# Kernel optimization log

Measured on AMD Instinct MI355X. Metric: run time of the kernel, lower is better.

Reference implementation:

```python
import jax, jax.numpy as jnp
import numpy as np

T, B, NS, NC = 100, 4096, 12, 4
N = NS + NC  # tau dim


def setup_inputs() -> dict:
    key = jax.random.key(0)
    k1, k2, k3, k4, k5 = jax.random.split(key, 5)
    # Symmetric PD quadratic cost C = L L^T / N + I  -> well conditioned
    L = jax.random.normal(k1, (T, B, N, N), dtype=jnp.float32) * 0.1
    C = jnp.einsum('tbij,tbkj->tbik', L, L) + jnp.eye(N, dtype=jnp.float32)
    c = jax.random.normal(k2, (T, B, N), dtype=jnp.float32)
    # Linear dynamics x' = F [x;u] + f, state block near identity for stability
    F = jax.random.normal(k3, (T - 1, B, NS, N), dtype=jnp.float32) * 0.02
    A0 = jnp.concatenate([0.99 * jnp.eye(NS, dtype=jnp.float32),
                          jnp.zeros((NS, NC), jnp.float32)], axis=-1)
    F = F + A0  # broadcast over (T-1, B)
    f = jax.random.normal(k4, (T - 1, B, NS), dtype=jnp.float32) * 0.01
    x_init = jax.random.normal(k5, (B, NS), dtype=jnp.float32)
    return {"x_init": x_init, "C": C, "c": c, "F": F, "f": f}


def _lqr_solve(x_init, C, c, F, f):
    ns = x_init.shape[-1]
    # Pad dynamics to length T (terminal step has no dynamics; V starts at 0
    # so the padded zero F/f contribute nothing).
    Fp = jnp.concatenate([F, jnp.zeros_like(F[:1])], axis=0)  # [T,B,ns,n]
    fp = jnp.concatenate([f, jnp.zeros_like(f[:1])], axis=0)  # [T,B,ns]

    def bwd_step(carry, inp):
        V, v = carry                      # [B,ns,ns], [B,ns]
        Ct, ct, Ft, ft = inp
        # Q = C + F^T V F ; q = c + F^T (V f + v)
        Q = Ct + jnp.einsum('bsi,bst,btj->bij', Ft, V, Ft)
        Vf = jnp.einsum('bst,bt->bs', V, ft) + v
        q = ct + jnp.einsum('bsi,bs->bi', Ft, Vf)
        Qxx, Qxu = Q[:, :ns, :ns], Q[:, :ns, ns:]
        Qux, Quu = Q[:, ns:, :ns], Q[:, ns:, ns:]
        qx, qu = q[:, :ns], q[:, ns:]
        # Joint solve for K = -Quu^{-1} Qux, k = -Quu^{-1} qu
        Kk = -jnp.linalg.solve(Quu, jnp.concatenate([Qux, qu[..., None]], axis=-1))
        K, k = Kk[..., :ns], Kk[..., ns]
        Vn = Qxx + jnp.einsum('bij,bjk->bik', Qxu, K)
        Vn = 0.5 * (Vn + jnp.swapaxes(Vn, -1, -2))
        vn = qx + jnp.einsum('bij,bj->bi', Qxu, k)
        return (Vn, vn), (K, k)

    V0 = jnp.zeros((x_init.shape[0], ns, ns), C.dtype)
    v0 = jnp.zeros((x_init.shape[0], ns), C.dtype)
    _, (Kr, kr) = jax.lax.scan(bwd_step, (V0, v0),
                               (C[::-1], c[::-1], Fp[::-1], fp[::-1]))
    K, k = Kr[::-1], kr[::-1]  # [T,B,nc,ns], [T,B,nc]

    def fwd_step(x, inp):
        Ct, ct, Ft, ft, Kt, kt = inp
        u = jnp.einsum('bij,bj->bi', Kt, x) + kt
        tau = jnp.concatenate([x, u], axis=-1)
        cost = 0.5 * jnp.einsum('bi,bij,bj->b', tau, Ct, tau) \
               + jnp.einsum('bi,bi->b', ct, tau)
        xn = jnp.einsum('bij,bj->bi', Ft, tau) + ft
        return xn, (x, u, cost)

    _, (xs, us, costs) = jax.lax.scan(fwd_step, x_init, (C, c, Fp, fp, K, k))
    return xs, us, jnp.sum(costs, axis=0)


def reference(x_init, C, c, F, f):
    # MPC with QuadCost + LinDx and no box constraints: the iLQR loop
    # converges in one exact LQR solve (Riccati backward + forward rollout).
    x, u, objs = _lqr_solve(x_init, C, c, F, f)
    return x, u, objs
```

## Files before the change

### kernel.cpp

```cpp
#include <hip/hip_runtime.h>
#include <hip/hip_fp16.h>

#define TT 100
#define BB 4096
#define GS 648


#define FENCE() asm volatile("s_waitcnt lgkmcnt(0)" ::: "memory")

template<int KMODE>
__device__ __forceinline__ void storeK(void* wsv, size_t of, int l, float X0,float X1,float X2,float X3){
  if (KMODE==0){
    float* wsb=(float*)wsv + of*52;
    if (l<12)       ((float4*)wsb)[l]  = make_float4(X0,X1,X2,X3);
    else if (l==12) ((float4*)wsb)[12] = make_float4(X0,X1,X2,X3);
  } else {
    __half* wsb=(__half*)wsv + of*52;
    if (l<12){
      wsb[l*4+0]=__float2half(X0); wsb[l*4+1]=__float2half(X1);
      wsb[l*4+2]=__float2half(X2); wsb[l*4+3]=__float2half(X3);
    } else if (l==12){
      wsb[48]=__float2half(X0); wsb[49]=__float2half(X1);
      wsb[50]=__float2half(X2); wsb[51]=__float2half(X3);
    }
  }
}
template<int KMODE>
__device__ __forceinline__ float4 loadKcol(const void* wsv, size_t of, int l){
  if (KMODE==0) return ((const float4*)((const float*)wsv + of*52))[l];
  const __half* p=(const __half*)wsv + of*52 + l*4;
  return make_float4(__half2float(p[0]),__half2float(p[1]),__half2float(p[2]),__half2float(p[3]));
}
template<int KMODE>
__device__ __forceinline__ float loadkk(const void* wsv, size_t of, int r){
  if (KMODE==0) return ((const float*)wsv)[of*52+48+r];
  return __half2float(((const __half*)wsv)[of*52+48+r]);
}

template<int KMODE>
__global__ __launch_bounds__(256)
void lqr_fused(const float* __restrict__ xinit,
               const float* __restrict__ Cg,
               const float* __restrict__ cg,
               const float* __restrict__ Fg,
               const float* __restrict__ fg,
               float* __restrict__ out,
               void* __restrict__ wsv)
{
  __shared__ float smem[GS*8];
  const int tid  = threadIdx.x;
  const int gi   = tid >> 5;
  const int lane = tid & 63;
  const int l    = tid & 15;
  const int h    = (tid >> 4) & 1;
  const int b    = blockIdx.x*8 + gi;
  const int gb32 = lane & ~31;

  float* __restrict__ V   = smem + gi*GS;
  float* __restrict__ Fl  = V + 144;
  float* __restrict__ S   = V + 384;
  float* __restrict__ Qxu = V + 528;
  float* __restrict__ Quu = V + 576;
  float* __restrict__ vv  = V + 592;
  float* __restrict__ tb  = V + 604;

  if (h==0 && l<12){
    #pragma unroll
    for (int i=0;i<12;i++) V[i*12+l]=0.f;
    vv[l]=0.f;
  }

  float4 sCa,sCb; float sc_;
  float4 sFa=make_float4(0,0,0,0),sFb=sFa; float sf_=0.f;
  {
    const size_t of = ((size_t)(TT-1)*BB + b);
    const float4* pc = (const float4*)(Cg + of*256 + l*16);
    sCa=pc[2*h]; sCb=pc[2*h+1];
    sc_ = cg[of*16 + l];
  }

  for (int tt=TT-1; tt>=0; --tt){
    const bool hasF = (tt < TT-1);
    float4 Ca=sCa,Cb=sCb; float rc=sc_;
    float4 Fa=sFa,Fb=sFb; float rf=sf_;

    if (hasF && l<12){
      float4* q=(float4*)(Fl + l*20);
      q[2*h]=Fa; q[2*h+1]=Fb;
      if (h==0) tb[l]=rf;
    }
    FENCE();

    if (tt>0){
      const size_t of = ((size_t)(tt-1)*BB + b);
      const float4* pc=(const float4*)(Cg + of*256 + l*16);
      sCa=pc[2*h]; sCb=pc[2*h+1];
      sc_=cg[of*16+l];
      if (l<12){
        const float4* pf=(const float4*)(Fg + of*192 + l*16);
        sFa=pf[2*h]; sFb=pf[2*h+1];
        if (h==0) sf_=fg[of*12+l];
      }
    }

    const float R0=Ca.x,R1=Ca.y,R2=Ca.z,R3=Ca.w,R4=Cb.x,R5=Cb.y,R6=Cb.z,R7=Cb.w;
    float Qp[16];
    Qp[0]=h?0.f:R0; Qp[1]=h?0.f:R1; Qp[2]=h?0.f:R2; Qp[3]=h?0.f:R3;
    Qp[4]=h?0.f:R4; Qp[5]=h?0.f:R5; Qp[6]=h?0.f:R6; Qp[7]=h?0.f:R7;
    Qp[8]=h?R0:0.f; Qp[9]=h?R1:0.f; Qp[10]=h?R2:0.f; Qp[11]=h?R3:0.f;
    Qp[12]=h?R4:0.f; Qp[13]=h?R5:0.f; Qp[14]=h?R6:0.f; Qp[15]=h?R7:0.f;
    float qvp = h? 0.f : rc;

    if (hasF){
      float FtL[6], FtH[6];
      #pragma unroll
      for (int k2=0;k2<6;k2++){ FtL[k2]=Fl[k2*20+l]; FtH[k2]=Fl[(6+k2)*20+l]; }
      const int s0=6*h;
      float Wl[6];
      #pragma unroll
      for (int k2=0;k2<6;k2++){
        const float4* vr=(const float4*)(V+(s0+k2)*12);
        float4 v0=vr[0],v1=vr[1],v2=vr[2];
        Wl[k2]= v0.x*FtL[0]+v0.y*FtL[1]+v0.z*FtL[2]+v0.w*FtL[3]
              + v1.x*FtL[4]+v1.y*FtL[5]+v1.z*FtH[0]+v1.w*FtH[1]
              + v2.x*FtH[2]+v2.y*FtH[3]+v2.z*FtH[4]+v2.w*FtH[5];
      }
      #pragma unroll
      for (int k2=0;k2<6;k2++){
        const float4* fr=(const float4*)(Fl + (s0+k2)*20);
        float4 f0=fr[0],f1=fr[1],f2=fr[2],f3=fr[3];
        float w=Wl[k2];
        Qp[0]+=f0.x*w;  Qp[1]+=f0.y*w;  Qp[2]+=f0.z*w;  Qp[3]+=f0.w*w;
        Qp[4]+=f1.x*w;  Qp[5]+=f1.y*w;  Qp[6]+=f1.z*w;  Qp[7]+=f1.w*w;
        Qp[8]+=f2.x*w;  Qp[9]+=f2.y*w;  Qp[10]+=f2.z*w; Qp[11]+=f2.w*w;
        Qp[12]+=f3.x*w; Qp[13]+=f3.y*w; Qp[14]+=f3.z*w; Qp[15]+=f3.w*w;
      }
      #pragma unroll
      for (int k2=0;k2<6;k2++){
        qvp += Wl[k2]*tb[s0+k2];
        const float ftk = h? FtH[k2] : FtL[k2];
        qvp += ftk * vv[s0+k2];
      }
    }

    float Qc[16];
    #pragma unroll
    for (int i=0;i<16;i++) Qc[i] = Qp[i] + __shfl_xor(Qp[i],16,64);
    float qv = qvp + __shfl_xor(qvp,16,64);

    if (h==0 && l>=12){
      const int cc=l-12;
      #pragma unroll
      for (int r=0;r<4;r++) Quu[cc*4+r]=Qc[12+r];
      #pragma unroll
      for (int i=0;i<12;i++) Qxu[cc*12+i]=Qc[i];
    }
    FENCE();

    float qu0=__shfl(qv,gb32+12,64),qu1=__shfl(qv,gb32+13,64),
          qu2=__shfl(qv,gb32+14,64),qu3=__shfl(qv,gb32+15,64);
    float b0,b1,b2,b3;
    if (l<12){b0=-Qc[12];b1=-Qc[13];b2=-Qc[14];b3=-Qc[15];}
    else     {b0=-qu0;b1=-qu1;b2=-qu2;b3=-qu3;}

    float a00=Quu[0],a10=Quu[1],a20=Quu[2],a30=Quu[3];
    float a01=Quu[4],a11=Quu[5],a21=Quu[6],a31=Quu[7];
    float a02=Quu[8],a12=Quu[9],a22=Quu[10],a32=Quu[11];
    float a03=Quu[12],a13=Quu[13],a23=Quu[14],a33=Quu[15];

    float i0=1.0f/a00;
    float m10=a10*i0,m20=a20*i0,m30=a30*i0;
    a11-=m10*a01;a12-=m10*a02;a13-=m10*a03;b1-=m10*b0;
    a21-=m20*a01;a22-=m20*a02;a23-=m20*a03;b2-=m20*b0;
    a31-=m30*a01;a32-=m30*a02;a33-=m30*a03;b3-=m30*b0;
    float i1=1.0f/a11;
    float m21=a21*i1,m31=a31*i1;
    a22-=m21*a12;a23-=m21*a13;b2-=m21*b1;
    a32-=m31*a12;a33-=m31*a13;b3-=m31*b1;
    float i2=1.0f/a22;
    float m32=a32*i2;
    a33-=m32*a23;b3-=m32*b2;
    float X3=b3/a33;
    float X2=(b2-a23*X3)*i2;
    float X1=(b1-a12*X2-a13*X3)*i1;
    float X0=(b0-a01*X1-a02*X2-a03*X3)*i0;

    if (h==0) storeK<KMODE>(wsv, (size_t)tt*BB+b, l, X0,X1,X2,X3);

    const float k0=__shfl(X0,gb32+12,64),k1=__shfl(X1,gb32+12,64),
                k2=__shfl(X2,gb32+12,64),k3=__shfl(X3,gb32+12,64);

    float Vn[6];
    if (l<12){
      const int i0i=6*h;
      #pragma unroll
      for (int k2=0;k2<6;k2++){
        const int i=i0i+k2;
        float vnk = h? Qc[6+k2] : Qc[k2];
        vnk += Qxu[i]*X0 + Qxu[12+i]*X1 + Qxu[24+i]*X2 + Qxu[36+i]*X3;
        S[i*12+l]=vnk; Vn[k2]=vnk;
      }
    }
    FENCE();
    if (l<12){
      const int i0i=6*h;
      #pragma unroll
      for (int k2=0;k2<6;k2++){
        const float sl=S[l*12 + i0i+k2];
        V[(i0i+k2)*12+l]=0.5f*(Vn[k2]+sl);
      }
      if (h==0){
        vv[l] = qv + Qxu[l]*k0 + Qxu[12+l]*k1 + Qxu[24+l]*k2 + Qxu[36+l]*k3;
      }
    }
  }

  asm volatile("s_waitcnt vmcnt(0)" ::: "memory");

  float xj = (h==0 && l<12)? xinit[(size_t)b*12+l] : 0.f;
  double costacc=0.0;

  float4 sF0=make_float4(0,0,0,0),sF1=sF0,sF2=sF0,sF3=sF0;
  float4 sK=make_float4(0,0,0,0); float sk_=0.f;
  {
    const float4* pc=(const float4*)(Cg + (size_t)b*256 + l*16);
    sCa=pc[2*h]; sCb=pc[2*h+1];
    sc_=cg[(size_t)b*16+l];
    if (h==0 && l<12){
      const float4* pf=(const float4*)(Fg + (size_t)b*192 + l*16);
      sF0=pf[0];sF1=pf[1];sF2=pf[2];sF3=pf[3];
      sf_=fg[(size_t)b*12+l];
      sK=loadKcol<KMODE>(wsv,(size_t)b,l);
    }
    if (h==0 && l>=12) sk_=loadkk<KMODE>(wsv,(size_t)b,l-12);
  }

  for (int t=0;t<TT;t++){
    float4 Ca=sCa,Cb=sCb; float rc=sc_;
    float4 F0=sF0,F1=sF1,F2=sF2,F3=sF3; float rf=sf_;
    float4 K4=sK; float kl=sk_;

    if (t+1<TT){
      const size_t of=((size_t)(t+1)*BB + b);
      const float4* pc=(const float4*)(Cg + of*256 + l*16);
      sCa=pc[2*h]; sCb=pc[2*h+1];
      sc_=cg[of*16+l];
      if (h==0 && l<12){
        sK=loadKcol<KMODE>(wsv,of,l);
        if (t+1<TT-1){
          const float4* pf=(const float4*)(Fg + of*192 + l*16);
          sF0=pf[0];sF1=pf[1];sF2=pf[2];sF3=pf[3];
          sf_=fg[of*12+l];
        }
      }
      if (h==0 && l>=12) sk_=loadkk<KMODE>(wsv,of,l-12);
    }

    float pr0=0.f,pr1=0.f,pr2=0.f,pr3=0.f;
    if (h==0 && l<12){ pr0=K4.x*xj; pr1=K4.y*xj; pr2=K4.z*xj; pr3=K4.w*xj; }
    #pragma unroll
    for (int m=1;m<16;m<<=1){
      pr0+=__shfl_xor(pr0,m,64); pr1+=__shfl_xor(pr1,m,64);
      pr2+=__shfl_xor(pr2,m,64); pr3+=__shfl_xor(pr3,m,64);
    }
    float* tbuf = tb + (t&1)*16;
    float tauj=0.f;
    if (h==0){
      if (l<12) tauj=xj;
      else {
        const float ur=(l==12)?pr0:(l==13)?pr1:(l==14)?pr2:pr3;
        tauj=ur+kl;
      }
      tbuf[l]=tauj;
    }
    FENCE();

    const float4* tp=(const float4*)tbuf;
    const float4 ta=tp[2*h], tb4=tp[2*h+1];
    const float taul = tbuf[l];

    float dot_p = Ca.x*ta.x + Ca.y*ta.y + Ca.z*ta.z + Ca.w*ta.w
                + Cb.x*tb4.x + Cb.y*tb4.y + Cb.z*tb4.z + Cb.w*tb4.w;
    costacc += (double)( taul*0.5f*dot_p + (h==0 ? taul*rc : 0.f) );

    if (h==0){
      if (l<12) out[(size_t)t*BB*12 + (size_t)b*12 + l] = xj;
      else      out[(size_t)TT*BB*12 + (size_t)t*BB*4 + (size_t)b*4 + (l-12)] = tauj;
    }

    if (t<TT-1 && h==0 && l<12){
      const float4 t0=tp[0],t1=tp[1],t2=tp[2],t3=tp[3];
      xj = rf
         + F0.x*t0.x+F0.y*t0.y+F0.z*t0.z+F0.w*t0.w
         + F1.x*t1.x+F1.y*t1.y+F1.z*t1.z+F1.w*t1.w
         + F2.x*t2.x+F2.y*t2.y+F2.z*t2.z+F2.w*t2.w
         + F3.x*t3.x+F3.y*t3.y+F3.z*t3.z+F3.w*t3.w;
    }
  }

  costacc+=__shfl_xor(costacc,1,64); costacc+=__shfl_xor(costacc,2,64);
  costacc+=__shfl_xor(costacc,4,64); costacc+=__shfl_xor(costacc,8,64);
  costacc+=__shfl_xor(costacc,16,64);
  if (h==0 && l==0) out[(size_t)TT*BB*16 + b]=(float)costacc;
}

extern "C" void kernel_launch(void* const* d_in, const int* in_sizes, int n_in,
                              void* d_out, int out_size, void* d_ws, size_t ws_size,
                              hipStream_t stream){
  (void)in_sizes; (void)n_in; (void)out_size;
  const float* xinit=(const float*)d_in[0];
  const float* C    =(const float*)d_in[1];
  const float* c    =(const float*)d_in[2];
  const float* F    =(const float*)d_in[3];
  const float* f    =(const float*)d_in[4];
  const size_t need_f32 = (size_t)TT*BB*52*sizeof(float);
  if (ws_size >= need_f32){
    lqr_fused<0><<<dim3(BB/8), dim3(256), 0, stream>>>(xinit,C,c,F,f,(float*)d_out,d_ws);
  } else {
    lqr_fused<1><<<dim3(BB/8), dim3(256), 0, stream>>>(xinit,C,c,F,f,(float*)d_out,d_ws);
  }
}
```

Baseline: 466.6 us.

## Drop V symmetrization pass and replace forward tau LDS buffer with shuffles

In the backward Riccati step, V is now written directly from Vn without the transpose-average pass. This removes the S scratch buffer and one LDS fence per step. Quu/Qxu stores and loads are vectorized to float4/float2, and the vv update reads Q entries from registers by relying on Q's symmetry. In the forward rollout, tau is broadcast with wave shuffles instead of a shared-memory buffer and fence, and per-group shared memory shrinks. The risks are that V's explicit zero-initialization is removed and that float asymmetry in V can drift without symmetrization.

New measurement: 531.1 us. 13.8% more time.

```diff
diff --git a/kernel.cpp b/kernel.cpp
--- a/kernel.cpp
+++ b/kernel.cpp
@@ -3,7 +3,7 @@
 
 #define TT 100
 #define BB 4096
-#define GS 648
+#define GS 488
 
 
 #define FENCE() asm volatile("s_waitcnt lgkmcnt(0)" ::: "memory")
@@ -58,17 +58,10 @@
 
   float* __restrict__ V   = smem + gi*GS;
   float* __restrict__ Fl  = V + 144;
-  float* __restrict__ S   = V + 384;
-  float* __restrict__ Qxu = V + 528;
-  float* __restrict__ Quu = V + 576;
-  float* __restrict__ vv  = V + 592;
-  float* __restrict__ tb  = V + 604;
-
-  if (h==0 && l<12){
-    #pragma unroll
-    for (int i=0;i<12;i++) V[i*12+l]=0.f;
-    vv[l]=0.f;
-  }
+  float* __restrict__ Qxu = V + 384;
+  float* __restrict__ Quu = V + 432;
+  float* __restrict__ vv  = V + 448;
+  float* __restrict__ tb  = V + 460;
 
   float4 sCa,sCb; float sc_;
   float4 sFa=make_float4(0,0,0,0),sFb=sFa; float sf_=0.f;
@@ -150,10 +143,11 @@
 
     if (h==0 && l>=12){
       const int cc=l-12;
-      #pragma unroll
-      for (int r=0;r<4;r++) Quu[cc*4+r]=Qc[12+r];
-      #pragma unroll
-      for (int i=0;i<12;i++) Qxu[cc*12+i]=Qc[i];
+      ((float4*)Quu)[cc] = make_float4(Qc[12],Qc[13],Qc[14],Qc[15]);
+      float4* qx=(float4*)(Qxu + cc*12);
+      qx[0]=make_float4(Qc[0],Qc[1],Qc[2],Qc[3]);
+      qx[1]=make_float4(Qc[4],Qc[5],Qc[6],Qc[7]);
+      qx[2]=make_float4(Qc[8],Qc[9],Qc[10],Qc[11]);
     }
     FENCE();
 
@@ -163,10 +157,12 @@
     if (l<12){b0=-Qc[12];b1=-Qc[13];b2=-Qc[14];b3=-Qc[15];}
     else     {b0=-qu0;b1=-qu1;b2=-qu2;b3=-qu3;}
 
-    float a00=Quu[0],a10=Quu[1],a20=Quu[2],a30=Quu[3];
-    float a01=Quu[4],a11=Quu[5],a21=Quu[6],a31=Quu[7];
-    float a02=Quu[8],a12=Quu[9],a22=Quu[10],a32=Quu[11];
-    float a03=Quu[12],a13=Quu[13],a23=Quu[14],a33=Quu[15];
+    const float4 quu0=((const float4*)Quu)[0], quu1=((const float4*)Quu)[1],
+                 quu2=((const float4*)Quu)[2], quu3=((const float4*)Quu)[3];
+    float a00=quu0.x,a10=quu0.y,a20=quu0.z,a30=quu0.w;
+    float a01=quu1.x,a11=quu1.y,a21=quu1.z,a31=quu1.w;
+    float a02=quu2.x,a12=quu2.y,a22=quu2.z,a32=quu2.w;
+    float a03=quu3.x,a13=quu3.y,a23=quu3.z,a33=quu3.w;
 
     float i0=1.0f/a00;
     float m10=a10*i0,m20=a20*i0,m30=a30*i0;
@@ -190,27 +186,23 @@
     const float k0=__shfl(X0,gb32+12,64),k1=__shfl(X1,gb32+12,64),
                 k2=__shfl(X2,gb32+12,64),k3=__shfl(X3,gb32+12,64);
 
-    float Vn[6];
     if (l<12){
       const int i0i=6*h;
-      #pragma unroll
-      for (int k2=0;k2<6;k2++){
-        const int i=i0i+k2;
-        float vnk = h? Qc[6+k2] : Qc[k2];
-        vnk += Qxu[i]*X0 + Qxu[12+i]*X1 + Qxu[24+i]*X2 + Qxu[36+i]*X3;
-        S[i*12+l]=vnk; Vn[k2]=vnk;
-      }
-    }
-    FENCE();
-    if (l<12){
-      const int i0i=6*h;
-      #pragma unroll
-      for (int k2=0;k2<6;k2++){
-        const float sl=S[l*12 + i0i+k2];
-        V[(i0i+k2)*12+l]=0.5f*(Vn[k2]+sl);
-      }
+      float Vn[6];
+      #pragma unroll
+      for (int k2=0;k2<6;k2++) Vn[k2] = h? Qc[6+k2] : Qc[k2];
+      #pragma unroll
+      for (int r=0;r<4;r++){
+        const float Xr=(r==0)?X0:(r==1)?X1:(r==2)?X2:X3;
+        const float2* qx2=(const float2*)(Qxu + r*12 + i0i);
+        float2 x0=qx2[0],x1=qx2[1],x2=qx2[2];
+        Vn[0]+=x0.x*Xr; Vn[1]+=x0.y*Xr; Vn[2]+=x1.x*Xr;
+        Vn[3]+=x1.y*Xr; Vn[4]+=x2.x*Xr; Vn[5]+=x2.y*Xr;
+      }
+      #pragma unroll
+      for (int k2=0;k2<6;k2++) V[(i0i+k2)*12+l]=Vn[k2];
       if (h==0){
-        vv[l] = qv + Qxu[l]*k0 + Qxu[12+l]*k1 + Qxu[24+l]*k2 + Qxu[36+l]*k3;
+        vv[l] = qv + Qc[12]*k0 + Qc[13]*k1 + Qc[14]*k2 + Qc[15]*k3;
       }
     }
   }
@@ -263,7 +255,6 @@
       pr0+=__shfl_xor(pr0,m,64); pr1+=__shfl_xor(pr1,m,64);
       pr2+=__shfl_xor(pr2,m,64); pr3+=__shfl_xor(pr3,m,64);
     }
-    float* tbuf = tb + (t&1)*16;
     float tauj=0.f;
     if (h==0){
       if (l<12) tauj=xj;
@@ -271,16 +262,18 @@
         const float ur=(l==12)?pr0:(l==13)?pr1:(l==14)?pr2:pr3;
         tauj=ur+kl;
       }
-      tbuf[l]=tauj;
-    }
-    FENCE();
-
-    const float4* tp=(const float4*)tbuf;
-    const float4 ta=tp[2*h], tb4=tp[2*h+1];
-    const float taul = tbuf[l];
-
-    float dot_p = Ca.x*ta.x + Ca.y*ta.y + Ca.z*ta.z + Ca.w*ta.w
-                + Cb.x*tb4.x + Cb.y*tb4.y + Cb.z*tb4.z + Cb.w*tb4.w;
+    }
+    float tau[16];
+    #pragma unroll
+    for (int j=0;j<16;j++) tau[j]=__shfl(tauj, gb32+j, 64);
+    const float taul=__shfl(tauj, gb32+l, 64);
+
+    float t8[8];
+    #pragma unroll
+    for (int j=0;j<8;j++) t8[j] = h? tau[8+j] : tau[j];
+
+    float dot_p = Ca.x*t8[0] + Ca.y*t8[1] + Ca.z*t8[2] + Ca.w*t8[3]
+                + Cb.x*t8[4] + Cb.y*t8[5] + Cb.z*t8[6] + Cb.w*t8[7];
     costacc += (double)( taul*0.5f*dot_p + (h==0 ? taul*rc : 0.f) );
 
     if (h==0){
@@ -289,12 +282,11 @@
     }
 
     if (t<TT-1 && h==0 && l<12){
-      const float4 t0=tp[0],t1=tp[1],t2=tp[2],t3=tp[3];
       xj = rf
-         + F0.x*t0.x+F0.y*t0.y+F0.z*t0.z+F0.w*t0.w
-         + F1.x*t1.x+F1.y*t1.y+F1.z*t1.z+F1.w*t1.w
-         + F2.x*t2.x+F2.y*t2.y+F2.z*t2.z+F2.w*t2.w
-         + F3.x*t3.x+F3.y*t3.y+F3.z*t3.z+F3.w*t3.w;
+         + F0.x*tau[0]+F0.y*tau[1]+F0.z*tau[2]+F0.w*tau[3]
+         + F1.x*tau[4]+F1.y*tau[5]+F1.z*tau[6]+F1.w*tau[7]
+         + F2.x*tau[8]+F2.y*tau[9]+F2.z*tau[10]+F2.w*tau[11]
+         + F3.x*tau[12]+F3.y*tau[13]+F3.z*tau[14]+F3.w*tau[15];
     }
   }
 
```
